# Kernel tuning notes

Measured on AMD Instinct MI355X. Metric: run time of the kernel, lower is better.

Reference implementation:

```python
import jax, jax.numpy as jnp
import numpy as np
from jax import lax

B, IMG, PATCH, INNER = 8, 224, 16, 4
EMB, MLP_DEPTH, DEPTH, HEADS = 512, 3, 24, 8
Hp = Wp = IMG // PATCH            # 14
N = Hp * Wp                       # 196
D4, D8 = EMB // 4, EMB // 2       # 128, 256
RPE_L = (2 * Hp - 1) * (2 * Wp - 1)  # 729
EPS = 1e-5


def _ln(x, g, b):
    m = jnp.mean(x, -1, keepdims=True)
    v = jnp.mean(jnp.square(x - m), -1, keepdims=True)
    return (x - m) * lax.rsqrt(v + EPS) * g + b


def _mlp(x, w1, b1, w2, b2):
    return jax.nn.gelu(x @ w1 + b1, approximate=False) @ w2 + b2


def _merge(x, ng, nb, rw):
    # merge 2x2 inner patches: dim -> 4*dim, then project to 2*dim
    x = jnp.concatenate([x[..., 0::2, 0::2, :], x[..., 1::2, 0::2, :],
                         x[..., 0::2, 1::2, :], x[..., 1::2, 1::2, :]], axis=-1)
    return _ln(x, ng, nb) @ rw


def _rpe_index():
    coords = np.stack(np.meshgrid(np.arange(Hp), np.arange(Wp), indexing='ij')).reshape(2, -1)
    rel = (coords[:, :, None] - coords[:, None, :]).transpose(1, 2, 0).astype(np.int64)
    rel[:, :, 0] += Hp - 1
    rel[:, :, 1] += Wp - 1
    rel[:, :, 0] *= 2 * Wp - 1
    return jnp.asarray(rel.sum(-1), dtype=jnp.int32)  # [N, N]


def setup_inputs():
    key = jax.random.key(0)
    cnt = [0]
    def rnd(shape, s=0.02):
        cnt[0] += 1
        return jax.random.normal(jax.random.fold_in(key, cnt[0]), shape, jnp.float32) * s
    d = {}
    d['image'] = jax.random.normal(jax.random.fold_in(key, 999), (B, 3, IMG, IMG), jnp.float32)
    d['conv_w'] = rnd((D4, 3, 4, 4)); d['conv_b'] = jnp.zeros((D4,), jnp.float32)
    d['pn_g'] = jnp.ones((D4,), jnp.float32); d['pn_b'] = jnp.zeros((D4,), jnp.float32)
    for pre, dim in (('s1', D4), ('s2', D8)):
        h = dim * 3  # bridge_mlp_ratio = 3
        d[pre + '_ng'] = jnp.ones((MLP_DEPTH, dim), jnp.float32)
        d[pre + '_nb'] = jnp.zeros((MLP_DEPTH, dim), jnp.float32)
        d[pre + '_w1'] = rnd((MLP_DEPTH, dim, h)); d[pre + '_b1'] = jnp.zeros((MLP_DEPTH, h), jnp.float32)
        d[pre + '_w2'] = rnd((MLP_DEPTH, h, dim)); d[pre + '_b2'] = jnp.zeros((MLP_DEPTH, dim), jnp.float32)
    d['pm1_ng'] = jnp.ones((4 * D4,), jnp.float32); d['pm1_nb'] = jnp.zeros((4 * D4,), jnp.float32); d['pm1_rw'] = rnd((4 * D4, 2 * D4))
    d['pm2_ng'] = jnp.ones((4 * D8,), jnp.float32); d['pm2_nb'] = jnp.zeros((4 * D8,), jnp.float32); d['pm2_rw'] = rnd((4 * D8, 2 * D8))
    d['ape'] = rnd((1, N, EMB))
    d['mb_n1g'] = jnp.ones((DEPTH, EMB), jnp.float32); d['mb_n1b'] = jnp.zeros((DEPTH, EMB), jnp.float32)
    d['mb_qkvw'] = rnd((DEPTH, EMB, 3 * EMB)); d['mb_qkvb'] = jnp.zeros((DEPTH, 3 * EMB), jnp.float32)
    d['mb_tab'] = rnd((DEPTH, RPE_L, HEADS))
    d['mb_projw'] = rnd((DEPTH, EMB, EMB)); d['mb_projb'] = jnp.zeros((DEPTH, EMB), jnp.float32)
    d['mb_n2g'] = jnp.ones((DEPTH, EMB), jnp.float32); d['mb_n2b'] = jnp.zeros((DEPTH, EMB), jnp.float32)
    d['mb_w1'] = rnd((DEPTH, EMB, 4 * EMB)); d['mb_b1'] = jnp.zeros((DEPTH, 4 * EMB), jnp.float32)
    d['mb_w2'] = rnd((DEPTH, 4 * EMB, EMB)); d['mb_b2'] = jnp.zeros((DEPTH, EMB), jnp.float32)
    d['rpe_index'] = _rpe_index()
    return d


def _forward(image, conv_w, conv_b, pn_g, pn_b,
             s1_ng, s1_nb, s1_w1, s1_b1, s1_w2, s1_b2,
             pm1_ng, pm1_nb, pm1_rw,
             s2_ng, s2_nb, s2_w1, s2_b1, s2_w2, s2_b2,
             pm2_ng, pm2_nb, pm2_rw, ape,
             mb_n1g, mb_n1b, mb_qkvw, mb_qkvb, mb_tab, mb_projw, mb_projb,
             mb_n2g, mb_n2b, mb_w1, mb_b1, mb_w2, mb_b2, rpe_index):
    # PatchEmbed: 4x4/4 conv then split into 16x16 patches of 4x4 inner patches
    x = lax.conv_general_dilated(image, conv_w, (4, 4), 'VALID',
                                 dimension_numbers=('NCHW', 'OIHW', 'NCHW'))
    x = x + conv_b[None, :, None, None]                       # [B, D4, 56, 56]
    b = x.shape[0]
    x = x.reshape(b, D4, Hp, INNER, Wp, INNER).transpose(0, 2, 4, 3, 5, 1)
    x = x.reshape(b, N, INNER, INNER, D4)
    x = _ln(x, pn_g, pn_b)

    def mlp_step(h, p):
        ng, nb, w1, b1, w2, b2 = p
        return h + _mlp(_ln(h, ng, nb), w1, b1, w2, b2), None

    x, _ = lax.scan(mlp_step, x, (s1_ng, s1_nb, s1_w1, s1_b1, s1_w2, s1_b2))
    x = _merge(x, pm1_ng, pm1_nb, pm1_rw)                     # inner 2x2, dim 256
    x, _ = lax.scan(mlp_step, x, (s2_ng, s2_nb, s2_w1, s2_b1, s2_w2, s2_b2))
    x = _merge(x, pm2_ng, pm2_nb, pm2_rw)                     # inner 1x1, dim 512
    x = x.reshape(b, N, EMB) + ape                            # absolute pos embed

    hd = EMB // HEADS
    scale = hd ** -0.5
    f32 = jnp.finfo(jnp.float32)

    def attn_step(h, p):
        n1g, n1b, qw, qb, tab, pw, pb, n2g, n2b, w1, b1, w2, b2 = p
        y = _ln(h, n1g, n1b)
        qkv = (y @ qw + qb).reshape(b, N, 3, HEADS, hd).transpose(2, 0, 3, 1, 4)
        q, k, v = qkv[0] * scale, qkv[1], qkv[2]
        bias = tab[rpe_index].transpose(2, 0, 1)              # [H, N, N] rpe gather
        a = jnp.einsum('bhqd,bhkd->bhqk', q, k) + bias[None]
        a = jnp.clip(a.astype(jnp.float32), f32.min, f32.max)
        a = jax.nn.softmax(a, axis=-1).astype(h.dtype)
        y = jnp.einsum('bhqk,bhkd->bhqd', a, v).transpose(0, 2, 1, 3).reshape(b, N, EMB)
        h = h + (y @ pw + pb)
        h = h + _mlp(_ln(h, n2g, n2b), w1, b1, w2, b2)
        return h, None

    x, _ = lax.scan(attn_step, x, (mb_n1g, mb_n1b, mb_qkvw, mb_qkvb, mb_tab,
                                   mb_projw, mb_projb, mb_n2g, mb_n2b,
                                   mb_w1, mb_b1, mb_w2, mb_b2))
    return x


def reference(image, conv_w, conv_b, pn_g, pn_b,
              s1_ng, s1_nb, s1_w1, s1_b1, s1_w2, s1_b2,
              pm1_ng, pm1_nb, pm1_rw,
              s2_ng, s2_nb, s2_w1, s2_b1, s2_w2, s2_b2,
              pm2_ng, pm2_nb, pm2_rw, ape,
              mb_n1g, mb_n1b, mb_qkvw, mb_qkvb, mb_tab, mb_projw, mb_projb,
              mb_n2g, mb_n2b, mb_w1, mb_b1, mb_w2, mb_b2, rpe_index):
    return _forward(image, conv_w, conv_b, pn_g, pn_b,
                    s1_ng, s1_nb, s1_w1, s1_b1, s1_w2, s1_b2,
                    pm1_ng, pm1_nb, pm1_rw,
                    s2_ng, s2_nb, s2_w1, s2_b1, s2_w2, s2_b2,
                    pm2_ng, pm2_nb, pm2_rw, ape,
                    mb_n1g, mb_n1b, mb_qkvw, mb_qkvb, mb_tab, mb_projw, mb_projb,
                    mb_n2g, mb_n2b, mb_w1, mb_b1, mb_w2, mb_b2, rpe_index)
```

## Files before the change

### kernel.cpp

```cpp
#include <hip/hip_runtime.h>
#include <hip/hip_bf16.h>

#define Bb    8
#define IMG   224
#define Hp    14
#define Np    196
#define D4    128
#define D8    256
#define EMB   512
#define HEADS 8
#define RPEL  729
#define DEPTH 24
#define EPS   1e-5f

constexpr int EPI_NONE = 0, EPI_BIAS = 1, EPI_BIAS_GELU = 2, EPI_BIAS_RES = 3, EPI_ATOMIC = 4, EPI_APE = 5;

typedef __bf16 bf16x8 __attribute__((ext_vector_type(8)));
typedef float  f32x4  __attribute__((ext_vector_type(4)));

static __device__ __forceinline__ void gload16(const void* g, void* l) {
    __builtin_amdgcn_global_load_lds(
        (const __attribute__((address_space(1))) void*)g,
        (__attribute__((address_space(3))) void*)l, 16, 0, 0);
}

__global__ __launch_bounds__(128) void conv_ln_kernel(
    const float* __restrict__ img, const float* __restrict__ cw,
    const float* __restrict__ cb,  const float* __restrict__ png,
    const float* __restrict__ pnb, float* __restrict__ xout)
{
    int p = blockIdx.x;
    int b = p / 3136, rem = p % 3136;
    int hh = rem / 56, ww = rem % 56;
    __shared__ float win[48];
    __shared__ float red[4];
    int t = threadIdx.x;
    if (t < 48) {
        int ic = t >> 4, kh = (t >> 2) & 3, kw = t & 3;
        win[t] = img[(((size_t)b*3 + ic)*224 + hh*4 + kh)*224 + ww*4 + kw];
    }
    __syncthreads();
    float acc = cb[t];
    const float* wrow = cw + (size_t)t * 48;
    #pragma unroll
    for (int r = 0; r < 48; ++r) acc += win[r] * wrow[r];
    float s = acc, ss = acc * acc;
    #pragma unroll
    for (int o = 32; o > 0; o >>= 1) { s += __shfl_xor(s, o, 64); ss += __shfl_xor(ss, o, 64); }
    int wv = t >> 6;
    if ((t & 63) == 0) { red[wv*2] = s; red[wv*2+1] = ss; }
    __syncthreads();
    s = red[0] + red[2]; ss = red[1] + red[3];
    float mean = s * (1.f/128.f);
    float rstd = rsqrtf(ss * (1.f/128.f) - mean*mean + EPS);
    float v = (acc - mean) * rstd * png[t] + pnb[t];
    int hp = hh >> 2, ih = hh & 3, wp = ww >> 2, iw = ww & 3;
    int bn = b * Np + hp * Hp + wp;
    xout[((size_t)bn*16 + ih*4 + iw)*128 + t] = v;
}

__global__ __launch_bounds__(256) void ln_kernel(
    const float* __restrict__ x, const float* __restrict__ g,
    const float* __restrict__ b, __bf16* __restrict__ y, int M, int D)
{
    int wave = threadIdx.x >> 6, lane = threadIdx.x & 63;
    int row = blockIdx.x * 4 + wave;
    if (row >= M) return;
    const float* xr = x + (size_t)row * D;
    float s = 0.f, ss = 0.f;
    for (int i = lane; i < D; i += 64) { float v = xr[i]; s += v; ss += v*v; }
    #pragma unroll
    for (int o = 32; o > 0; o >>= 1) { s += __shfl_xor(s, o, 64); ss += __shfl_xor(ss, o, 64); }
    float inv = 1.f / (float)D;
    float mean = s * inv;
    float rstd = rsqrtf(ss * inv - mean*mean + EPS);
    __bf16* yr = y + (size_t)row * D;
    for (int i = lane; i < D; i += 64)
        yr[i] = (__bf16)((xr[i] - mean) * rstd * g[i] + b[i]);
}

__global__ __launch_bounds__(256) void merge1_ln_kernel(
    const float* __restrict__ x, const float* __restrict__ g,
    const float* __restrict__ b, __bf16* __restrict__ y)
{
    int wave = threadIdx.x >> 6, lane = threadIdx.x & 63;
    int row = blockIdx.x * 4 + wave;
    if (row >= 6272) return;
    int j2 = row & 1, i2 = (row >> 1) & 1, bn = row >> 2;
    float vals[8]; float s = 0.f, ss = 0.f;
    #pragma unroll
    for (int t = 0; t < 8; ++t) {
        int e = lane + t*64;
        int k = e >> 7, c = e & 127;
        int ih = 2*i2 + (k & 1), iw = 2*j2 + (k >> 1);
        float v = x[((size_t)bn*16 + ih*4 + iw)*128 + c];
        vals[t] = v; s += v; ss += v*v;
    }
    #pragma unroll
    for (int o = 32; o > 0; o >>= 1) { s += __shfl_xor(s, o, 64); ss += __shfl_xor(ss, o, 64); }
    float mean = s * (1.f/512.f);
    float rstd = rsqrtf(ss * (1.f/512.f) - mean*mean + EPS);
    __bf16* yr = y + (size_t)row * 512;
    #pragma unroll
    for (int t = 0; t < 8; ++t) {
        int e = lane + t*64;
        yr[e] = (__bf16)((vals[t] - mean) * rstd * g[e] + b[e]);
    }
}

__global__ __launch_bounds__(256) void merge2_ln_kernel(
    const float* __restrict__ x, const float* __restrict__ g,
    const float* __restrict__ b, __bf16* __restrict__ y)
{
    int wave = threadIdx.x >> 6, lane = threadIdx.x & 63;
    int row = blockIdx.x * 4 + wave;
    if (row >= 1568) return;
    float vals[16]; float s = 0.f, ss = 0.f;
    #pragma unroll
    for (int t = 0; t < 16; ++t) {
        int e = lane + t*64;
        int k = e >> 8, c = e & 255;
        float v = x[((size_t)row*4 + (k & 1)*2 + (k >> 1))*256 + c];
        vals[t] = v; s += v; ss += v*v;
    }
    #pragma unroll
    for (int o = 32; o > 0; o >>= 1) { s += __shfl_xor(s, o, 64); ss += __shfl_xor(ss, o, 64); }
    float mean = s * (1.f/1024.f);
    float rstd = rsqrtf(ss * (1.f/1024.f) - mean*mean + EPS);
    __bf16* yr = y + (size_t)row * 1024;
    #pragma unroll
    for (int t = 0; t < 16; ++t) {
        int e = lane + t*64;
        yr[e] = (__bf16)((vals[t] - mean) * rstd * g[e] + b[e]);
    }
}

static __device__ __forceinline__ void tconv_tile(
    const float* __restrict__ in, __bf16* __restrict__ out,
    int R, int C, int tile, float (*t)[33])
{
    int tiles_c = C >> 5;
    int tr = tile / tiles_c, tc = tile - tr * tiles_c;
    int ty = threadIdx.x >> 3, tx = threadIdx.x & 7;
    const float4 v = *(const float4*)&in[(size_t)(tr*32 + ty) * C + (tc*32 + tx*4)];
    t[ty][tx*4+0] = v.x; t[ty][tx*4+1] = v.y; t[ty][tx*4+2] = v.z; t[ty][tx*4+3] = v.w;
    __syncthreads();
    __bf16 o[4];
    #pragma unroll
    for (int j = 0; j < 4; ++j) o[j] = (__bf16)t[tx*4+j][ty];
    *(uint2*)&out[(size_t)(tc*32 + ty) * R + (tr*32 + tx*4)] = *(const uint2*)o;
}

__global__ __launch_bounds__(256) void tconv_kernel(
    const float* __restrict__ in, __bf16* __restrict__ out, int R, int C)
{
    __shared__ float t[32][33];
    size_t off = (size_t)blockIdx.y * R * C;
    tconv_tile(in + off, out + off, R, C, blockIdx.x, t);
}

static __device__ __forceinline__ void tconv64_tile(
    const float* __restrict__ in, __bf16* __restrict__ out,
    int R, int C, int tile, float (*t)[65])
{
    int tiles_c = C >> 6;
    int tr = tile / tiles_c, tc = tile - tr * tiles_c;
    int tid = threadIdx.x;
    int lrow = tid >> 4, lcol = (tid & 15) << 2;
    #pragma unroll
    for (int i = 0; i < 4; ++i) {
        int row = lrow + i*16;
        const float4 v = *(const float4*)&in[(size_t)(tr*64 + row) * C + (tc*64 + lcol)];
        t[row][lcol+0] = v.x; t[row][lcol+1] = v.y; t[row][lcol+2] = v.z; t[row][lcol+3] = v.w;
    }
    __syncthreads();
    int orow = tid >> 3, och = tid & 7;
    #pragma unroll
    for (int i = 0; i < 2; ++i) {
        int r = orow + i*32;
        __bf16 o[8];
        #pragma unroll
        for (int j = 0; j < 8; ++j) o[j] = (__bf16)t[och*8 + j][r];
        *(uint4*)&out[(size_t)(tc*64 + r) * R + (tr*64 + och*8)] = *(const uint4*)o;
    }
}

__global__ __launch_bounds__(256) void layer_tconv_kernel(
    const float* __restrict__ qkvw, const float* __restrict__ projw,
    const float* __restrict__ w1, const float* __restrict__ w2,
    __bf16* __restrict__ LW, size_t lw_stride)
{
    __shared__ float t[64][65];
    int l = blockIdx.y;
    int b = blockIdx.x;
    const float* q_ = qkvw  + (size_t)l * 786432;
    const float* p_ = projw + (size_t)l * 262144;
    const float* a_ = w1    + (size_t)l * 1048576;
    const float* c_ = w2    + (size_t)l * 1048576;
    __bf16* o = LW + (size_t)l * lw_stride;
    if (b < 192)       tconv64_tile(q_, o,           512, 1536, b,       t);
    else if (b < 256)  tconv64_tile(p_, o +  786432, 512,  512, b - 192, t);
    else if (b < 512)  tconv64_tile(a_, o + 1048576, 512, 2048, b - 256, t);
    else               tconv64_tile(c_, o + 2097152, 2048, 512, b - 512, t);
}

template<int BM, int EPI>
__global__ __launch_bounds__(256) void gemm_kernel(
    const __bf16* __restrict__ A, const __bf16* __restrict__ Bt,
    const float* __restrict__ bias, const float* __restrict__ Rres,
    void* __restrict__ Cv, int M, int N, int K, int kChunk)
{
    constexpr int BF = (BM == 128) ? 4 : 2;
    __shared__ __bf16 As[BM][32];
    __shared__ __bf16 Bs[128][32];
    const int tid = threadIdx.x, lane = tid & 63, wave = tid >> 6;
    const int m0 = blockIdx.y * BM, n0 = blockIdx.x << 7;
    int wm, wn;
    if constexpr (BM == 128) { wm = (wave >> 1) << 6; wn = (wave & 1) << 6; }
    else                     { wm = 0;                wn = wave << 5;       }
    const int q = lane >> 4, mr = lane & 15;
    const int kstart = blockIdx.z * kChunk;
    const int kend   = min(kstart + kChunk, K);

    f32x4 acc[4][BF];
    #pragma unroll
    for (int i = 0; i < 4; ++i)
        #pragma unroll
        for (int j = 0; j < BF; ++j)
            acc[i][j] = (f32x4){0.f, 0.f, 0.f, 0.f};

    const int crow = tid >> 2, ccol = (tid & 3) << 3;
    const __bf16* ag0 = A + (size_t)min(m0 + crow, M - 1) * K + ccol;
    const __bf16* ag1 = ag0;
    if constexpr (BM == 128)
        ag1 = A + (size_t)min(m0 + 64 + crow, M - 1) * K + ccol;
    const __bf16* bg0 = Bt + (size_t)(n0 + crow) * K + ccol;
    const __bf16* bg1 = Bt + (size_t)(n0 + 64 + crow) * K + ccol;
    char* lA = (char*)&As[0][0] + wave * 1024;
    char* lB = (char*)&Bs[0][0] + wave * 1024;

    for (int k0 = kstart; k0 < kend; k0 += 32) {
        gload16(ag0 + k0, lA);
        if constexpr (BM == 128) gload16(ag1 + k0, lA + 4096);
        gload16(bg0 + k0, lB);
        gload16(bg1 + k0, lB + 4096);
        __syncthreads();
        bf16x8 af[4], bfr[BF];
        #pragma unroll
        for (int i = 0; i < 4; ++i)
            af[i] = *(const bf16x8*)&As[wm + i*16 + mr][q*8];
        #pragma unroll
        for (int j = 0; j < BF; ++j)
            bfr[j] = *(const bf16x8*)&Bs[wn + j*16 + mr][q*8];
        #pragma unroll
        for (int i = 0; i < 4; ++i)
            #pragma unroll
            for (int j = 0; j < BF; ++j)
                acc[i][j] = __builtin_amdgcn_mfma_f32_16x16x32_bf16(af[i], bfr[j], acc[i][j], 0, 0, 0);
        __syncthreads();
    }

    const bool addb = (blockIdx.z == 0);
    #pragma unroll
    for (int i = 0; i < 4; ++i) {
        #pragma unroll
        for (int j = 0; j < BF; ++j) {
            const int n = n0 + wn + j*16 + mr;
            float bv = 0.f;
            if constexpr (EPI != EPI_NONE) bv = bias[n];
            #pragma unroll
            for (int r = 0; r < 4; ++r) {
                const int m = m0 + wm + i*16 + q*4 + r;
                if (m < M) {
                    if constexpr (EPI == EPI_ATOMIC) {
                        atomicAdd(&((float*)Cv)[(size_t)m * N + n], acc[i][j][r] + (addb ? bv : 0.f));
                    } else {
                        float v = acc[i][j][r] + bv;
                        if constexpr (EPI == EPI_BIAS_GELU)
                            v = 0.5f * v * (1.f + erff(v * 0.70710678118654752f));
                        if constexpr (EPI == EPI_BIAS_RES)
                            v += Rres[(size_t)m * N + n];
                        if constexpr (EPI == EPI_BIAS || EPI == EPI_BIAS_GELU)
                            ((__bf16*)Cv)[(size_t)m * N + n] = (__bf16)v;
                        else
                            ((float*)Cv)[(size_t)m * N + n] = v;
                    }
                }
            }
        }
    }
}

template<int EPI>
__global__ __launch_bounds__(256) void gemm64_kernel(
    const __bf16* __restrict__ A, const __bf16* __restrict__ Bt,
    const float* __restrict__ bias, const float* __restrict__ Rres,
    void* __restrict__ Cv, int M, int N, int K, int kChunk)
{
    __shared__ __bf16 As[64][64];
    __shared__ __bf16 Bs[64][64];
    const int tid = threadIdx.x, lane = tid & 63, wave = tid >> 6;
    const int m0 = blockIdx.y << 6, n0 = blockIdx.x << 6;
    const int wm = (wave >> 1) << 5, wn = (wave & 1) << 5;
    const int q = lane >> 4, mr = lane & 15;
    const int kstart = blockIdx.z * kChunk;
    const int kend   = min(kstart + kChunk, K);

    f32x4 acc[2][2];
    #pragma unroll
    for (int i = 0; i < 2; ++i)
        #pragma unroll
        for (int j = 0; j < 2; ++j)
            acc[i][j] = (f32x4){0.f, 0.f, 0.f, 0.f};

    const int srow = tid >> 3;
    const int scol = ((tid & 7) << 3) ^ ((srow & 7) << 3);
    const __bf16* agA = A  + (size_t)min(m0 + srow,      M - 1) * K + scol;
    const __bf16* agB = A  + (size_t)min(m0 + 32 + srow, M - 1) * K + scol;
    const __bf16* bgA = Bt + (size_t)(n0 + srow)      * K + scol;
    const __bf16* bgB = Bt + (size_t)(n0 + 32 + srow) * K + scol;
    char* lA = (char*)&As[0][0] + wave * 1024;
    char* lB = (char*)&Bs[0][0] + wave * 1024;

    const int pg0 = ((q)     ^ (mr & 7)) << 4;
    const int pg1 = ((q + 4) ^ (mr & 7)) << 4;

    for (int k0 = kstart; k0 < kend; k0 += 64) {
        gload16(agA + k0, lA);
        gload16(agB + k0, lA + 4096);
        gload16(bgA + k0, lB);
        gload16(bgB + k0, lB + 4096);
        __syncthreads();
        bf16x8 af[2][2], bfr[2][2];
        #pragma unroll
        for (int i = 0; i < 2; ++i) {
            const char* ar = (const char*)&As[wm + i*16 + mr][0];
            af[i][0] = *(const bf16x8*)(ar + pg0);
            af[i][1] = *(const bf16x8*)(ar + pg1);
        }
        #pragma unroll
        for (int j = 0; j < 2; ++j) {
            const char* br = (const char*)&Bs[wn + j*16 + mr][0];
            bfr[j][0] = *(const bf16x8*)(br + pg0);
            bfr[j][1] = *(const bf16x8*)(br + pg1);
        }
        #pragma unroll
        for (int i = 0; i < 2; ++i)
            #pragma unroll
            for (int j = 0; j < 2; ++j) {
                acc[i][j] = __builtin_amdgcn_mfma_f32_16x16x32_bf16(af[i][0], bfr[j][0], acc[i][j], 0, 0, 0);
                acc[i][j] = __builtin_amdgcn_mfma_f32_16x16x32_bf16(af[i][1], bfr[j][1], acc[i][j], 0, 0, 0);
            }
        __syncthreads();
    }

    const bool addb = (blockIdx.z == 0);
    #pragma unroll
    for (int i = 0; i < 2; ++i) {
        #pragma unroll
        for (int j = 0; j < 2; ++j) {
            const int n = n0 + wn + j*16 + mr;
            float bv = 0.f;
            if constexpr (EPI == EPI_BIAS || EPI == EPI_BIAS_GELU || EPI == EPI_BIAS_RES || EPI == EPI_ATOMIC)
                bv = bias[n];
            #pragma unroll
            for (int r = 0; r < 4; ++r) {
                const int m = m0 + wm + i*16 + q*4 + r;
                if (m < M) {
                    if constexpr (EPI == EPI_ATOMIC) {
                        atomicAdd(&((float*)Cv)[(size_t)m * N + n], acc[i][j][r] + (addb ? bv : 0.f));
                    } else {
                        float v = acc[i][j][r] + bv;
                        if constexpr (EPI == EPI_BIAS_GELU)
                            v = 0.5f * v * (1.f + erff(v * 0.70710678118654752f));
                        if constexpr (EPI == EPI_BIAS_RES)
                            v += Rres[(size_t)m * N + n];
                        if constexpr (EPI == EPI_APE)
                            v += Rres[(size_t)(m % Np) * N + n];
                        if constexpr (EPI == EPI_BIAS || EPI == EPI_BIAS_GELU)
                            ((__bf16*)Cv)[(size_t)m * N + n] = (__bf16)v;
                        else
                            ((float*)Cv)[(size_t)m * N + n] = v;
                    }
                }
            }
        }
    }
}

__global__ __launch_bounds__(256) void attn_kernel(
    const __bf16* __restrict__ qkv, const float* __restrict__ tab,
    const int* __restrict__ rpe, __bf16* __restrict__ y2)
{
    __shared__ __bf16 Vt[64][232];
    __shared__ __bf16 Pl[4][16][232];
    int blk = blockIdx.x;
    int qg = blk & 3, h = (blk >> 2) & 7, b = blk >> 5;
    int tid = threadIdx.x;

    for (int i = tid; i < 196*8; i += 256) {
        int key = i >> 3, seg = i & 7;
        bf16x8 v = *(const bf16x8*)(qkv + ((size_t)(b*Np + key))*1536 + 1024 + h*64 + seg*8);
        #pragma unroll
        for (int j = 0; j < 8; ++j) Vt[seg*8 + j][key] = v[j];
    }
    {
        int d0 = tid >> 2, cs = tid & 3;
        #pragma unroll
        for (int j = 0; j < 9; ++j) Vt[d0][196 + cs*9 + j] = (__bf16)0.f;
    }
    __syncthreads();

    int lane = tid & 63, wave = tid >> 6;
    int T = qg + 4*wave;
    if (T > 12) return;
    int q = lane >> 4, mr = lane & 15;

    if (lane < 36) {
        #pragma unroll
        for (int r = 0; r < 16; ++r) Pl[wave][r][196 + lane] = (__bf16)0.f;
    }

    int qtok = b*Np + min(T*16 + mr, 195);
    const __bf16* qp = qkv + (size_t)qtok*1536 + h*64 + q*8;
    bf16x8 aq0 = *(const bf16x8*)qp;
    bf16x8 aq1 = *(const bf16x8*)(qp + 32);

    f32x4 sacc[13];
    #pragma unroll
    for (int nt = 0; nt < 13; ++nt) {
        int ktok = b*Np + min(nt*16 + mr, 195);
        const __bf16* kp = qkv + (size_t)ktok*1536 + 512 + h*64 + q*8;
        bf16x8 bk0 = *(const bf16x8*)kp;
        bf16x8 bk1 = *(const bf16x8*)(kp + 32);
        f32x4 z = (f32x4){0.f, 0.f, 0.f, 0.f};
        z = __builtin_amdgcn_mfma_f32_16x16x32_bf16(aq0, bk0, z, 0, 0, 0);
        sacc[nt] = __builtin_amdgcn_mfma_f32_16x16x32_bf16(aq1, bk1, z, 0, 0, 0);
    }

    #pragma unroll
    for (int r = 0; r < 4; ++r) {
        int qi = T*16 + q*4 + r;
        const int* rrow = rpe + (size_t)min(qi, 195) * 196;
        float vals[13];
        #pragma unroll
        for (int nt = 0; nt < 13; ++nt) {
            int col = nt*16 + mr;
            float bv = tab[rrow[min(col, 195)]*8 + h];
            float v = sacc[nt][r] * 0.125f + bv;
            vals[nt] = (col < 196) ? v : -3.0e38f;
        }
        float m = vals[0];
        #pragma unroll
        for (int nt = 1; nt < 13; ++nt) m = fmaxf(m, vals[nt]);
        #pragma unroll
        for (int o = 8; o > 0; o >>= 1) m = fmaxf(m, __shfl_xor(m, o, 64));
        float s = 0.f, p[13];
        #pragma unroll
        for (int nt = 0; nt < 13; ++nt) { p[nt] = __expf(vals[nt] - m); s += p[nt]; }
        #pragma unroll
        for (int o = 8; o > 0; o >>= 1) s += __shfl_xor(s, o, 64);
        float inv = 1.f / s;
        #pragma unroll
        for (int nt = 0; nt < 13; ++nt)
            Pl[wave][q*4 + r][nt*16 + mr] = (__bf16)(p[nt] * inv);
    }

    f32x4 oacc[4];
    #pragma unroll
    for (int nt = 0; nt < 4; ++nt) oacc[nt] = (f32x4){0.f, 0.f, 0.f, 0.f};
    #pragma unroll
    for (int ks = 0; ks < 7; ++ks) {
        bf16x8 ap = *(const bf16x8*)&Pl[wave][mr][ks*32 + q*8];
        #pragma unroll
        for (int nt = 0; nt < 4; ++nt) {
            bf16x8 bv = *(const bf16x8*)&Vt[nt*16 + mr][ks*32 + q*8];
            oacc[nt] = __builtin_amdgcn_mfma_f32_16x16x32_bf16(ap, bv, oacc[nt], 0, 0, 0);
        }
    }

    #pragma unroll
    for (int nt = 0; nt < 4; ++nt) {
        #pragma unroll
        for (int r = 0; r < 4; ++r) {
            int qi = T*16 + q*4 + r;
            if (qi < 196)
                y2[((size_t)(b*Np + qi))*512 + h*64 + nt*16 + mr] = (__bf16)oacc[nt][r];
        }
    }
}

extern "C" void kernel_launch(void* const* d_in, const int* in_sizes, int n_in,
                              void* d_out, int out_size, void* d_ws, size_t ws_size,
                              hipStream_t stream)
{
    typedef const float* fp;
    fp image  = (fp)d_in[0];
    fp conv_w = (fp)d_in[1];  fp conv_b = (fp)d_in[2];
    fp pn_g   = (fp)d_in[3];  fp pn_b   = (fp)d_in[4];
    fp s1_ng  = (fp)d_in[5];  fp s1_nb  = (fp)d_in[6];
    fp s1_w1  = (fp)d_in[7];  fp s1_b1  = (fp)d_in[8];
    fp s1_w2  = (fp)d_in[9];  fp s1_b2  = (fp)d_in[10];
    fp s2_ng  = (fp)d_in[11]; fp s2_nb  = (fp)d_in[12];
    fp s2_w1  = (fp)d_in[13]; fp s2_b1  = (fp)d_in[14];
    fp s2_w2  = (fp)d_in[15]; fp s2_b2  = (fp)d_in[16];
    fp pm1_ng = (fp)d_in[17]; fp pm1_nb = (fp)d_in[18]; fp pm1_rw = (fp)d_in[19];
    fp pm2_ng = (fp)d_in[20]; fp pm2_nb = (fp)d_in[21]; fp pm2_rw = (fp)d_in[22];
    fp ape    = (fp)d_in[23];
    fp n1g    = (fp)d_in[24]; fp n1b    = (fp)d_in[25];
    fp qkvw   = (fp)d_in[26]; fp qkvb   = (fp)d_in[27];
    fp tab    = (fp)d_in[28];
    fp projw  = (fp)d_in[29]; fp projb  = (fp)d_in[30];
    fp n2g    = (fp)d_in[31]; fp n2b    = (fp)d_in[32];
    fp w1     = (fp)d_in[33]; fp b1     = (fp)d_in[34];
    fp w2     = (fp)d_in[35]; fp b2     = (fp)d_in[36];
    const int* rpe = (const int*)d_in[37];

    float*  X  = (float*)d_ws;
    __bf16* H  = (__bf16*)(X + 3211264);
    __bf16* Y  = H + 9633792;
    __bf16* SW = Y + 3211264;
    __bf16* LW = SW + 2129920;

    const size_t LWSTRIDE = 3145728;
    const size_t need_all = ((size_t)(LW - (__bf16*)d_ws)) * 2 + DEPTH * LWSTRIDE * 2;
    const bool bigLW = ws_size >= need_all;

    tconv_kernel<<<dim3(48, 3),  256, 0, stream>>>(s1_w1,  SW + 0,       128, 384);
    tconv_kernel<<<dim3(48, 3),  256, 0, stream>>>(s1_w2,  SW + 147456,  384, 128);
    tconv_kernel<<<dim3(192, 3), 256, 0, stream>>>(s2_w1,  SW + 294912,  256, 768);
    tconv_kernel<<<dim3(192, 3), 256, 0, stream>>>(s2_w2,  SW + 884736,  768, 256);
    tconv_kernel<<<dim3(128, 1), 256, 0, stream>>>(pm1_rw, SW + 1474560, 512, 256);
    tconv_kernel<<<dim3(512, 1), 256, 0, stream>>>(pm2_rw, SW + 1605632, 1024, 512);
    if (bigLW)
        layer_tconv_kernel<<<dim3(768, DEPTH), 256, 0, stream>>>(
            qkvw, projw, w1, w2, LW, LWSTRIDE);

    conv_ln_kernel<<<Bb*56*56, 128, 0, stream>>>(image, conv_w, conv_b, pn_g, pn_b, X);

    for (int t = 0; t < 3; ++t) {
        ln_kernel<<<25088/4, 256, 0, stream>>>(X, s1_ng + t*128, s1_nb + t*128, Y, 25088, 128);
        gemm_kernel<128, EPI_BIAS_GELU><<<dim3(3, 196), 256, 0, stream>>>(
            Y, SW + t*49152, s1_b1 + t*384, nullptr, H, 25088, 384, 128, 128);
        gemm_kernel<64, EPI_BIAS_RES><<<dim3(1, 392), 256, 0, stream>>>(
            H, SW + 147456 + t*49152, s1_b2 + t*128, X, X, 25088, 128, 384, 384);
    }
    merge1_ln_kernel<<<6272/4, 256, 0, stream>>>(X, pm1_ng, pm1_nb, Y);
    gemm64_kernel<EPI_NONE><<<dim3(4, 98), 256, 0, stream>>>(
        Y, SW + 1474560, nullptr, nullptr, X, 6272, 256, 512, 512);
    for (int t = 0; t < 3; ++t) {
        ln_kernel<<<6272/4, 256, 0, stream>>>(X, s2_ng + t*256, s2_nb + t*256, Y, 6272, 256);
        gemm_kernel<128, EPI_BIAS_GELU><<<dim3(6, 49), 256, 0, stream>>>(
            Y, SW + 294912 + t*196608, s2_b1 + t*768, nullptr, H, 6272, 768, 256, 256);
        gemm_kernel<64, EPI_BIAS_RES><<<dim3(2, 98), 256, 0, stream>>>(
            H, SW + 884736 + t*196608, s2_b2 + t*256, X, X, 6272, 256, 768, 768);
    }
    merge2_ln_kernel<<<1568/4, 256, 0, stream>>>(X, pm2_ng, pm2_nb, Y);
    gemm64_kernel<EPI_APE><<<dim3(8, 25), 256, 0, stream>>>(
        Y, SW + 1605632, nullptr, ape, X, 1568, 512, 1024, 1024);

    for (int l = 0; l < DEPTH; ++l) {
        const __bf16* LWl = bigLW ? LW + (size_t)l * LWSTRIDE : LW;
        if (!bigLW)
            layer_tconv_kernel<<<dim3(768, 1), 256, 0, stream>>>(
                qkvw + (size_t)l*512*1536, projw + (size_t)l*512*512,
                w1 + (size_t)l*512*2048, w2 + (size_t)l*2048*512, LW, 0);
        ln_kernel<<<392, 256, 0, stream>>>(X, n1g + l*EMB, n1b + l*EMB, Y, 1568, EMB);
        gemm64_kernel<EPI_BIAS><<<dim3(24, 25), 256, 0, stream>>>(
            Y, LWl, qkvb + (size_t)l*1536, nullptr, H, 1568, 1536, EMB, EMB);
        attn_kernel<<<256, 256, 0, stream>>>(H, tab + (size_t)l*RPEL*HEADS, rpe, Y);
        gemm64_kernel<EPI_ATOMIC><<<dim3(8, 25, 4), 256, 0, stream>>>(
            Y, LWl + 786432, projb + (size_t)l*EMB, nullptr, X, 1568, EMB, EMB, 128);
        ln_kernel<<<392, 256, 0, stream>>>(X, n2g + l*EMB, n2b + l*EMB, Y, 1568, EMB);
        gemm64_kernel<EPI_BIAS_GELU><<<dim3(32, 25), 256, 0, stream>>>(
            Y, LWl + 1048576, b1 + (size_t)l*2048, nullptr, H, 1568, 2048, EMB, EMB);
        gemm64_kernel<EPI_ATOMIC><<<dim3(8, 25, 4), 256, 0, stream>>>(
            H, LWl + 2097152, b2 + (size_t)l*EMB, nullptr, X, 1568, EMB, 2048, 512);
    }
    hipMemcpyAsync(d_out, X, (size_t)1568*512*sizeof(float), hipMemcpyDeviceToDevice, stream);
}
```

Baseline: 2.808 ms.

## Double-buffer LDS tiles in both GEMM kernels to overlap loads with MFMA

Both bf16 GEMM kernels now keep two LDS stages. Each iteration issues the global-to-LDS loads for the next K tile before running the MFMAs on the current one, then waits on vmcnt and a single barrier before swapping buffers. This hides global load latency behind compute and drops one barrier per iteration. In exchange it doubles LDS use per block, which can lower occupancy. It also relies on the compiler not reordering LDS reads past the inline waitcnt.

```diff
diff --git a/kernel.cpp b/kernel.cpp
--- a/kernel.cpp
+++ b/kernel.cpp
@@ -211,8 +211,10 @@
     void* __restrict__ Cv, int M, int N, int K, int kChunk)
 {
     constexpr int BF = (BM == 128) ? 4 : 2;
-    __shared__ __bf16 As[BM][32];
-    __shared__ __bf16 Bs[128][32];
+    constexpr int ABYTES = BM * 64;
+    constexpr int BBYTES = 8192;
+    __shared__ __bf16 As[2][BM][32];
+    __shared__ __bf16 Bs[2][128][32];
     const int tid = threadIdx.x, lane = tid & 63, wave = tid >> 6;
     const int m0 = blockIdx.y * BM, n0 = blockIdx.x << 7;
     int wm, wn;
@@ -236,29 +238,40 @@
         ag1 = A + (size_t)min(m0 + 64 + crow, M - 1) * K + ccol;
     const __bf16* bg0 = Bt + (size_t)(n0 + crow) * K + ccol;
     const __bf16* bg1 = Bt + (size_t)(n0 + 64 + crow) * K + ccol;
-    char* lA = (char*)&As[0][0] + wave * 1024;
-    char* lB = (char*)&Bs[0][0] + wave * 1024;
-
+    char* lA = (char*)&As[0][0][0] + wave * 1024;
+    char* lB = (char*)&Bs[0][0][0] + wave * 1024;
+
+#define STAGEB(k0_, buf_) do {                                        \
+        gload16(ag0 + (k0_), lA + (buf_) * ABYTES);                   \
+        if constexpr (BM == 128)                                      \
+            gload16(ag1 + (k0_), lA + (buf_) * ABYTES + 4096);        \
+        gload16(bg0 + (k0_), lB + (buf_) * BBYTES);                   \
+        gload16(bg1 + (k0_), lB + (buf_) * BBYTES + 4096);            \
+    } while (0)
+
+    STAGEB(kstart, 0);
+    asm volatile("s_waitcnt vmcnt(0)" ::: "memory");
+    __builtin_amdgcn_s_barrier();
+    int cur = 0;
     for (int k0 = kstart; k0 < kend; k0 += 32) {
-        gload16(ag0 + k0, lA);
-        if constexpr (BM == 128) gload16(ag1 + k0, lA + 4096);
-        gload16(bg0 + k0, lB);
-        gload16(bg1 + k0, lB + 4096);
-        __syncthreads();
+        if (k0 + 32 < kend) STAGEB(k0 + 32, cur ^ 1);
         bf16x8 af[4], bfr[BF];
         #pragma unroll
         for (int i = 0; i < 4; ++i)
-            af[i] = *(const bf16x8*)&As[wm + i*16 + mr][q*8];
+            af[i] = *(const bf16x8*)&As[cur][wm + i*16 + mr][q*8];
         #pragma unroll
         for (int j = 0; j < BF; ++j)
-            bfr[j] = *(const bf16x8*)&Bs[wn + j*16 + mr][q*8];
+            bfr[j] = *(const bf16x8*)&Bs[cur][wn + j*16 + mr][q*8];
         #pragma unroll
         for (int i = 0; i < 4; ++i)
             #pragma unroll
             for (int j = 0; j < BF; ++j)
                 acc[i][j] = __builtin_amdgcn_mfma_f32_16x16x32_bf16(af[i], bfr[j], acc[i][j], 0, 0, 0);
-        __syncthreads();
-    }
+        asm volatile("s_waitcnt vmcnt(0)" ::: "memory");
+        __builtin_amdgcn_s_barrier();
+        cur ^= 1;
+    }
+#undef STAGEB
 
     const bool addb = (blockIdx.z == 0);
     #pragma unroll
@@ -297,8 +310,8 @@
     const float* __restrict__ bias, const float* __restrict__ Rres,
     void* __restrict__ Cv, int M, int N, int K, int kChunk)
 {
-    __shared__ __bf16 As[64][64];
-    __shared__ __bf16 Bs[64][64];
+    __shared__ __bf16 As[2][64][64];
+    __shared__ __bf16 Bs[2][64][64];
     const int tid = threadIdx.x, lane = tid & 63, wave = tid >> 6;
     const int m0 = blockIdx.y << 6, n0 = blockIdx.x << 6;
     const int wm = (wave >> 1) << 5, wn = (wave & 1) << 5;
@@ -319,28 +332,35 @@
     const __bf16* agB = A  + (size_t)min(m0 + 32 + srow, M - 1) * K + scol;
     const __bf16* bgA = Bt + (size_t)(n0 + srow)      * K + scol;
     const __bf16* bgB = Bt + (size_t)(n0 + 32 + srow) * K + scol;
-    char* lA = (char*)&As[0][0] + wave * 1024;
-    char* lB = (char*)&Bs[0][0] + wave * 1024;
+    char* lA = (char*)&As[0][0][0] + wave * 1024;
+    char* lB = (char*)&Bs[0][0][0] + wave * 1024;
 
     const int pg0 = ((q)     ^ (mr & 7)) << 4;
     const int pg1 = ((q + 4) ^ (mr & 7)) << 4;
 
+#define STAGE64(k0_, buf_) do {                                       \
+        gload16(agA + (k0_), lA + (buf_) * 8192);                     \
+        gload16(agB + (k0_), lA + (buf_) * 8192 + 4096);              \
+        gload16(bgA + (k0_), lB + (buf_) * 8192);                     \
+        gload16(bgB + (k0_), lB + (buf_) * 8192 + 4096);              \
+    } while (0)
+
+    STAGE64(kstart, 0);
+    asm volatile("s_waitcnt vmcnt(0)" ::: "memory");
+    __builtin_amdgcn_s_barrier();
+    int cur = 0;
     for (int k0 = kstart; k0 < kend; k0 += 64) {
-        gload16(agA + k0, lA);
-        gload16(agB + k0, lA + 4096);
-        gload16(bgA + k0, lB);
-        gload16(bgB + k0, lB + 4096);
-        __syncthreads();
+        if (k0 + 64 < kend) STAGE64(k0 + 64, cur ^ 1);
         bf16x8 af[2][2], bfr[2][2];
         #pragma unroll
         for (int i = 0; i < 2; ++i) {
-            const char* ar = (const char*)&As[wm + i*16 + mr][0];
+            const char* ar = (const char*)&As[cur][wm + i*16 + mr][0];
             af[i][0] = *(const bf16x8*)(ar + pg0);
             af[i][1] = *(const bf16x8*)(ar + pg1);
         }
         #pragma unroll
         for (int j = 0; j < 2; ++j) {
-            const char* br = (const char*)&Bs[wn + j*16 + mr][0];
+            const char* br = (const char*)&Bs[cur][wn + j*16 + mr][0];
             bfr[j][0] = *(const bf16x8*)(br + pg0);
             bfr[j][1] = *(const bf16x8*)(br + pg1);
         }
@@ -351,8 +371,11 @@
                 acc[i][j] = __builtin_amdgcn_mfma_f32_16x16x32_bf16(af[i][0], bfr[j][0], acc[i][j], 0, 0, 0);
                 acc[i][j] = __builtin_amdgcn_mfma_f32_16x16x32_bf16(af[i][1], bfr[j][1], acc[i][j], 0, 0, 0);
             }
-        __syncthreads();
-    }
+        asm volatile("s_waitcnt vmcnt(0)" ::: "memory");
+        __builtin_amdgcn_s_barrier();
+        cur ^= 1;
+    }
+#undef STAGE64
 
     const bool addb = (blockIdx.z == 0);
     #pragma unroll
```

Result: no change. 2.808 ms (-0.0%).
